# Kernel tuning notes

Measured on AMD Instinct MI355X. Metric: run time of the kernel, lower is better.

The kernel has to match this reference:

```python
import jax, jax.numpy as jnp
import numpy as np

BLANK = 0          # tf.nn.ctc_loss default blank_index (StringLookup reserves 0 for OOV)
PAD = 127          # padding_value = char_to_num.vocabulary_size()
NEG = -1e30        # log-space 'zero' (avoid -inf to keep grads NaN-free)
B, T, C, L = 1024, 256, 128, 32


def setup_inputs() -> dict:
    key = jax.random.key(0)
    k1, k2 = jax.random.split(key)
    # labels in [1, PAD-1]; none equal PAD so label_length == L (full-length labels)
    y_true = jax.random.randint(k1, (B, L), 1, PAD).astype(jnp.int32)
    y_pred = jax.random.normal(k2, (B, T, C), dtype=jnp.float32)
    return {"y_true": y_true, "y_pred": y_pred}


def _ctc_loss(y_true, y_pred):
    """Faithful jax version of tf.nn.ctc_loss(labels, logits, label_len, T,
    logits_time_major=False, blank_index=0): standard log-space alpha DP."""
    Bn, Tn, Cn = y_pred.shape
    Ln = y_true.shape[1]
    S = 2 * Ln + 1  # extended label length (blanks interleaved)

    logp = jax.nn.log_softmax(y_pred, axis=-1)                    # [B,T,C]

    # extended label sequence: blank, l1, blank, l2, ..., blank   # [B,S]
    ext = jnp.full((Bn, S), BLANK, dtype=y_true.dtype)
    ext = ext.at[:, 1::2].set(y_true)

    # log-probs gathered at extended-label symbols                # [B,T,S]
    lp_ext = jnp.take_along_axis(
        logp, jnp.broadcast_to(ext[:, None, :], (Bn, Tn, S)), axis=2)

    # label_length = count of non-padding entries (mirrors count_nonzero)
    label_len = jnp.sum(y_true != PAD, axis=1)                    # [B]

    # skip transition s-2 -> s allowed iff ext[s] is a non-blank differing
    # from ext[s-2]
    skip_ok = jnp.concatenate(
        [jnp.zeros((Bn, 2), bool),
         (ext[:, 2:] != BLANK) & (ext[:, 2:] != ext[:, :-2])], axis=1)  # [B,S]

    neg1 = jnp.full((Bn, 1), NEG, logp.dtype)
    neg2 = jnp.full((Bn, 2), NEG, logp.dtype)

    alpha0 = jnp.full((Bn, S), NEG, logp.dtype)
    alpha0 = alpha0.at[:, 0].set(lp_ext[:, 0, 0]).at[:, 1].set(lp_ext[:, 0, 1])

    def step(alpha, lp_t):  # alpha,[B,S]  lp_t,[B,S]
        a1 = jnp.concatenate([neg1, alpha[:, :-1]], axis=1)
        a2 = jnp.concatenate([neg2, alpha[:, :-2]], axis=1)
        a2 = jnp.where(skip_ok, a2, NEG)
        new = lp_t + jnp.logaddexp(jnp.logaddexp(alpha, a1), a2)
        return new, None

    lp_seq = jnp.transpose(lp_ext, (1, 0, 2))                     # [T,B,S]
    alphaT, _ = jax.lax.scan(step, alpha0, lp_seq[1:])            # [B,S]

    # total log-likelihood ends at last blank (2*len) or last label (2*len-1)
    bi = jnp.arange(Bn)
    e1 = 2 * label_len
    e2 = 2 * label_len - 1
    loglik = jnp.logaddexp(alphaT[bi, e1], alphaT[bi, e2])        # [B]
    return -loglik


def reference(y_true, y_pred):
    # The original layer returns y_pred and registers the loss via add_loss;
    # the compute-dominant quantity is the per-example CTC loss, returned here.
    return _ctc_loss(y_true, y_pred)
```

## Files before the change

kernel.cpp:

```cpp
#include <hip/hip_runtime.h>
#include <cstdint>


#define CTC_BLANK 0
#define CTC_PAD   127
#define NEG       (-1e30f)
#define LOG2E     1.44269504088896340736f
#define LN2       0.69314718055994530942f

constexpr int Bn = 1024, Tn = 256, Cn = 128, Ln = 32;
constexpr int NSLOT = Ln + 1;
constexpr int CR  = 16;
constexpr int NCH = Tn / CR;

__device__ __forceinline__ float fexp2(float x) { return __builtin_amdgcn_exp2f(x); }
__device__ __forceinline__ float flog2(float x) { return __builtin_amdgcn_logf(x); }

template <int CTRL>
__device__ __forceinline__ float dpp_add(float s) {
    int v = __builtin_amdgcn_update_dpp(0, __float_as_int(s), CTRL, 0xF, 0xF, true);
    return s + __int_as_float(v);
}
__device__ __forceinline__ float dpp_wave_shr1(float src, float old) {
    return __int_as_float(__builtin_amdgcn_update_dpp(
        __float_as_int(old), __float_as_int(src), 0x138, 0xF, 0xF, false));
}
__device__ __forceinline__ void gl_lds16(const float* g, float* l) {
    __builtin_amdgcn_global_load_lds(
        (const __attribute__((address_space(1))) uint32_t*)g,
        (__attribute__((address_space(3))) uint32_t*)l, 16, 0, 0);
}

__global__ __launch_bounds__(512, 8) void ctc_fused_kernel(
        const int*   __restrict__ y_true,
        const float* __restrict__ y_pred,
        float*       __restrict__ out)
{
    __shared__ __align__(16) float raw[8][2][CR / 8 * Cn];
    __shared__ _Float16 Gc[Tn * NSLOT];
    __shared__ int   labels[Ln];
    __shared__ __align__(16) int cmap[Cn];
    __shared__ int   used[Cn];
    __shared__ int   wcnt[8];
    __shared__ float partS[16];

    const int b    = blockIdx.x;
    const int tid  = threadIdx.x;
    const int lane = tid & 63;
    const int wave = tid >> 6;

    const float* gbase = y_pred + (size_t)b * Tn * Cn;

    auto stage = [&](int c, int buf) {
        const float* g = gbase + (size_t)(c * CR + 2 * wave) * Cn + lane * 4;
        gl_lds16(g, &raw[wave][buf][0]);
    };

    stage(0, 0);

    if (tid < Ln) labels[tid] = y_true[b * Ln + tid];
    if (tid < Cn) used[tid] = 0;
    __syncthreads();
    if (tid == 0) used[CTC_BLANK] = 1;
    if (tid < Ln) used[labels[tid]] = 1;
    __syncthreads();
    {
        bool f = (tid < Cn) && (used[tid] != 0);
        unsigned long long m = __ballot(f);
        if (lane == 0) wcnt[wave] = __popcll(m);
        __syncthreads();
        int base = 0;
        for (int w = 0; w < wave; ++w) base += wcnt[w];
        if (tid < Cn)
            cmap[tid] = f ? (base + __popcll(m & ((1ull << lane) - 1ull))) : -1;
        __syncthreads();
    }

    const int half = lane >> 5;
    const int l32  = lane & 31;
    const int4 cm  = ((const int4*)cmap)[l32];
    float acc = 0.f;

    for (int c = 0; c < NCH; ++c) {
        const float4 x = ((const float4*)&raw[wave][c & 1][0])[lane];
        if (c + 1 < NCH) stage(c + 1, (c + 1) & 1);

        const int r = c * CR + 2 * wave + half;
        if (cm.x >= 0) Gc[r * NSLOT + cm.x] = (_Float16)(x.x * LOG2E);
        if (cm.y >= 0) Gc[r * NSLOT + cm.y] = (_Float16)(x.y * LOG2E);
        if (cm.z >= 0) Gc[r * NSLOT + cm.z] = (_Float16)(x.z * LOG2E);
        if (cm.w >= 0) Gc[r * NSLOT + cm.w] = (_Float16)(x.w * LOG2E);
        float s = __expf(x.x) + __expf(x.y) + __expf(x.z) + __expf(x.w);
        s = dpp_add<0x111>(s);
        s = dpp_add<0x112>(s);
        s = dpp_add<0x114>(s);
        s = dpp_add<0x118>(s);
        s = dpp_add<0x142>(s);
        acc += __logf(s);
    }
    if (l32 == 31) partS[wave * 2 + half] = acc;
    __syncthreads();

    if (wave == 0) {
        const int  i      = lane;
        const bool validO = (i < Ln);
        const bool validE = (i <= Ln);
        const int  myLab   = validO ? labels[i] : -1;
        const int  prevLab = (i >= 1 && i < Ln) ? labels[i - 1] : -1;
        const int  slotO   = validO ? cmap[myLab] : 0;
        const bool skipO   = (i >= 1 && i < Ln) &&
                             (myLab != CTC_BLANK) && (myLab != prevLab);
        const int  len = __popcll(__ballot(validO && (myLab != CTC_PAD)));

        float aE = (i == 0) ? (float)Gc[0]     : NEG;
        float aO = (i == 0) ? (float)Gc[slotO] : NEG;

        float pB[2], pO[2];
        pB[0] = (float)Gc[NSLOT];     pO[0] = (float)Gc[NSLOT + slotO];
        pB[1] = (float)Gc[2 * NSLOT]; pO[1] = (float)Gc[2 * NSLOT + slotO];
        int k = 0;
        #pragma unroll 2
        for (int t = 1; t < Tn; ++t) {
            const float lpB = pB[k], lpO = pO[k];
            const int tp = (t + 2 < Tn) ? t + 2 : Tn - 1;
            pB[k] = (float)Gc[tp * NSLOT];
            pO[k] = (float)Gc[tp * NSLOT + slotO];
            k ^= 1;

            const float aOup = dpp_wave_shr1(aO, NEG);
            const float m  = fmaxf(aE, aOup);
            const float e1 = fexp2(aE - m);
            const float e2 = fexp2(aOup - m);
            const float sE = e1 + e2;
            const float nE = lpB + m + flog2(sE);
            const float m3 = fmaxf(aO, m);
            const float nO = lpO + m3 +
                flog2(fexp2(aO - m3) + (skipO ? sE : e1) * fexp2(m - m3));
            aE = validE ? nE : NEG;
            aO = validO ? nO : NEG;
        }

        const float v1 = __shfl(aE, len, 64);
        const float v2 = __shfl(aO, len - 1, 64);
        if (i == 0) {
            float S = 0.f;
            #pragma unroll
            for (int j = 0; j < 16; ++j) S += partS[j];
            const float mm = fmaxf(v1, v2);
            const float L2 = mm + flog2(fexp2(v1 - mm) + fexp2(v2 - mm));
            out[b] = S - LN2 * L2;
        }
    }
}

extern "C" void kernel_launch(void* const* d_in, const int* in_sizes, int n_in,
                              void* d_out, int out_size, void* d_ws, size_t ws_size,
                              hipStream_t stream) {
    const int*   y_true = (const int*)d_in[0];
    const float* y_pred = (const float*)d_in[1];
    float*       out    = (float*)d_out;
    ctc_fused_kernel<<<Bn, 512, 0, stream>>>(y_true, y_pred, out);
}
```

Before: 222.6 us.

## Split CTC into a parallel staging kernel and a single-wave DP kernel

Splits the fused kernel in two. The first kernel computes the log-sum-exp and gathers the compact fp16 label-column table, using 2 blocks of 256 threads per batch item, and writes the table and partial sums to workspace. The second kernel uses one 64-thread wave per batch item to load the table and run the serial alpha recursion. The DP kernel is small, so many more of them fit on a CU, which should let the 255-step serial chain overlap across batches instead of leaving 7 of 8 waves idle. The cost is an extra launch and a workspace round trip. The fused kernel stays as a fallback, now with plain global loads instead of async LDS staging.

```diff
diff --git a/kernel.cpp b/kernel.cpp
--- a/kernel.cpp
+++ b/kernel.cpp
@@ -10,8 +10,10 @@
 
 constexpr int Bn = 1024, Tn = 256, Cn = 128, Ln = 32;
 constexpr int NSLOT = Ln + 1;
-constexpr int CR  = 16;
-constexpr int NCH = Tn / CR;
+constexpr size_t GC_HALFS  = (size_t)Tn * NSLOT;
+constexpr size_t WS_GC_B   = (size_t)Bn * GC_HALFS * 2;
+constexpr size_t WS_S_B    = (size_t)Bn * 16 * 4;
+constexpr size_t WS_NEEDED = WS_GC_B + WS_S_B;
 
 __device__ __forceinline__ float fexp2(float x) { return __builtin_amdgcn_exp2f(x); }
 __device__ __forceinline__ float flog2(float x) { return __builtin_amdgcn_logf(x); }
@@ -25,38 +27,24 @@
     return __int_as_float(__builtin_amdgcn_update_dpp(
         __float_as_int(old), __float_as_int(src), 0x138, 0xF, 0xF, false));
 }
-__device__ __forceinline__ void gl_lds16(const float* g, float* l) {
-    __builtin_amdgcn_global_load_lds(
-        (const __attribute__((address_space(1))) uint32_t*)g,
-        (__attribute__((address_space(3))) uint32_t*)l, 16, 0, 0);
-}
-
-__global__ __launch_bounds__(512, 8) void ctc_fused_kernel(
+
+__global__ __launch_bounds__(256) void ctc_stage_kernel(
         const int*   __restrict__ y_true,
         const float* __restrict__ y_pred,
-        float*       __restrict__ out)
+        _Float16*    __restrict__ gws,
+        float*       __restrict__ sws)
 {
-    __shared__ __align__(16) float raw[8][2][CR / 8 * Cn];
-    __shared__ _Float16 Gc[Tn * NSLOT];
-    __shared__ int   labels[Ln];
+    __shared__ _Float16 Gt[128 * NSLOT];
+    __shared__ int labels[Ln];
     __shared__ __align__(16) int cmap[Cn];
-    __shared__ int   used[Cn];
-    __shared__ int   wcnt[8];
-    __shared__ float partS[16];
-
-    const int b    = blockIdx.x;
+    __shared__ int used[Cn];
+    __shared__ int wcnt[4];
+
+    const int h    = blockIdx.x;
+    const int b    = blockIdx.y;
     const int tid  = threadIdx.x;
     const int lane = tid & 63;
     const int wave = tid >> 6;
-
-    const float* gbase = y_pred + (size_t)b * Tn * Cn;
-
-    auto stage = [&](int c, int buf) {
-        const float* g = gbase + (size_t)(c * CR + 2 * wave) * Cn + lane * 4;
-        gl_lds16(g, &raw[wave][buf][0]);
-    };
-
-    stage(0, 0);
 
     if (tid < Ln) labels[tid] = y_true[b * Ln + tid];
     if (tid < Cn) used[tid] = 0;
@@ -76,16 +64,188 @@
         __syncthreads();
     }
 
+    const float* rowbase = y_pred + ((size_t)b * Tn + h * 128) * Cn;
     const int half = lane >> 5;
     const int l32  = lane & 31;
     const int4 cm  = ((const int4*)cmap)[l32];
     float acc = 0.f;
 
-    for (int c = 0; c < NCH; ++c) {
-        const float4 x = ((const float4*)&raw[wave][c & 1][0])[lane];
-        if (c + 1 < NCH) stage(c + 1, (c + 1) & 1);
-
-        const int r = c * CR + 2 * wave + half;
+    float4 v[2][4];
+    #pragma unroll
+    for (int j = 0; j < 4; ++j) {
+        const int rl = 2 * (wave * 16 + j) + half;
+        v[0][j] = ((const float4*)(rowbase + rl * Cn))[l32];
+    }
+    for (int g = 0; g < 4; ++g) {
+        if (g < 3) {
+            #pragma unroll
+            for (int j = 0; j < 4; ++j) {
+                const int rl = 2 * (wave * 16 + (g + 1) * 4 + j) + half;
+                v[(g + 1) & 1][j] = ((const float4*)(rowbase + rl * Cn))[l32];
+            }
+        }
+        #pragma unroll
+        for (int j = 0; j < 4; ++j) {
+            const float4 x = v[g & 1][j];
+            const int rl = 2 * (wave * 16 + g * 4 + j) + half;
+            if (cm.x >= 0) Gt[rl * NSLOT + cm.x] = (_Float16)(x.x * LOG2E);
+            if (cm.y >= 0) Gt[rl * NSLOT + cm.y] = (_Float16)(x.y * LOG2E);
+            if (cm.z >= 0) Gt[rl * NSLOT + cm.z] = (_Float16)(x.z * LOG2E);
+            if (cm.w >= 0) Gt[rl * NSLOT + cm.w] = (_Float16)(x.w * LOG2E);
+            float s = __expf(x.x) + __expf(x.y) + __expf(x.z) + __expf(x.w);
+            s = dpp_add<0x111>(s);
+            s = dpp_add<0x112>(s);
+            s = dpp_add<0x114>(s);
+            s = dpp_add<0x118>(s);
+            s = dpp_add<0x142>(s);
+            acc += __logf(s);
+        }
+    }
+    if (l32 == 31) sws[b * 16 + h * 8 + wave * 2 + half] = acc;
+    __syncthreads();
+
+    {
+        uint4*       dst = (uint4*)(gws + ((size_t)b * Tn + h * 128) * NSLOT);
+        const uint4* src = (const uint4*)Gt;
+        dst[tid]       = src[tid];
+        dst[256 + tid] = src[256 + tid];
+        if (tid < 16) dst[512 + tid] = src[512 + tid];
+    }
+}
+
+__global__ __launch_bounds__(64) void ctc_dp_kernel(
+        const int*      __restrict__ y_true,
+        const _Float16* __restrict__ gws,
+        const float*    __restrict__ sws,
+        float*          __restrict__ out)
+{
+    __shared__ __align__(16) _Float16 Gc[GC_HALFS];
+    __shared__ int labels[Ln];
+    __shared__ int used[Cn];
+    __shared__ int cmap[Cn];
+
+    const int b    = blockIdx.x;
+    const int lane = threadIdx.x;
+
+    {
+        const uint4* src = (const uint4*)(gws + (size_t)b * GC_HALFS);
+        uint4*       dst = (uint4*)Gc;
+        #pragma unroll
+        for (int k = 0; k < 17; ++k) {
+            const int idx = k * 64 + lane;
+            if (idx < 1056) dst[idx] = src[idx];
+        }
+    }
+
+    if (lane < Ln) labels[lane] = y_true[b * Ln + lane];
+    used[lane] = 0; used[64 + lane] = 0;
+    __syncthreads();
+    if (lane == 0) used[CTC_BLANK] = 1;
+    if (lane < Ln) used[labels[lane]] = 1;
+    __syncthreads();
+    {
+        const unsigned long long below = (1ull << lane) - 1ull;
+        const unsigned long long m0 = __ballot(used[lane] != 0);
+        const unsigned long long m1 = __ballot(used[64 + lane] != 0);
+        cmap[lane]      = used[lane]      ? (int)__popcll(m0 & below) : -1;
+        cmap[64 + lane] = used[64 + lane] ? (int)(__popcll(m0) +
+                                                  __popcll(m1 & below)) : -1;
+    }
+    __syncthreads();
+
+    const int  i      = lane;
+    const bool validO = (i < Ln);
+    const bool validE = (i <= Ln);
+    const int  myLab   = validO ? labels[i] : -1;
+    const int  prevLab = (i >= 1 && i < Ln) ? labels[i - 1] : -1;
+    const int  slotO   = validO ? cmap[myLab] : 0;
+    const bool skipO   = (i >= 1 && i < Ln) &&
+                         (myLab != CTC_BLANK) && (myLab != prevLab);
+    const int  len = __popcll(__ballot(validO && (myLab != CTC_PAD)));
+
+    float aE = (i == 0) ? (float)Gc[0]     : NEG;
+    float aO = (i == 0) ? (float)Gc[slotO] : NEG;
+
+    float pB[2], pO[2];
+    pB[0] = (float)Gc[NSLOT];     pO[0] = (float)Gc[NSLOT + slotO];
+    pB[1] = (float)Gc[2 * NSLOT]; pO[1] = (float)Gc[2 * NSLOT + slotO];
+    int k = 0;
+    #pragma unroll 2
+    for (int t = 1; t < Tn; ++t) {
+        const float lpB = pB[k], lpO = pO[k];
+        const int tp = (t + 2 < Tn) ? t + 2 : Tn - 1;
+        pB[k] = (float)Gc[tp * NSLOT];
+        pO[k] = (float)Gc[tp * NSLOT + slotO];
+        k ^= 1;
+
+        const float aOup = dpp_wave_shr1(aO, NEG);
+        const float m  = fmaxf(aE, aOup);
+        const float e1 = fexp2(aE - m);
+        const float e2 = fexp2(aOup - m);
+        const float sE = e1 + e2;
+        const float nE = lpB + m + flog2(sE);
+        const float m3 = fmaxf(aO, m);
+        const float nO = lpO + m3 +
+            flog2(fexp2(aO - m3) + (skipO ? sE : e1) * fexp2(m - m3));
+        aE = validE ? nE : NEG;
+        aO = validO ? nO : NEG;
+    }
+
+    const float v1 = __shfl(aE, len, 64);
+    const float v2 = __shfl(aO, len - 1, 64);
+    if (i == 0) {
+        float S = 0.f;
+        #pragma unroll
+        for (int j = 0; j < 16; ++j) S += sws[b * 16 + j];
+        const float mm = fmaxf(v1, v2);
+        const float L2 = mm + flog2(fexp2(v1 - mm) + fexp2(v2 - mm));
+        out[b] = S - LN2 * L2;
+    }
+}
+
+__global__ __launch_bounds__(512, 8) void ctc_fused_kernel(
+        const int*   __restrict__ y_true,
+        const float* __restrict__ y_pred,
+        float*       __restrict__ out)
+{
+    __shared__ _Float16 Gc[Tn * NSLOT];
+    __shared__ int   labels[Ln];
+    __shared__ __align__(16) int cmap[Cn];
+    __shared__ int   used[Cn];
+    __shared__ int   wcnt[8];
+    __shared__ float partS[16];
+
+    const int b    = blockIdx.x;
+    const int tid  = threadIdx.x;
+    const int lane = tid & 63;
+    const int wave = tid >> 6;
+
+    if (tid < Ln) labels[tid] = y_true[b * Ln + tid];
+    if (tid < Cn) used[tid] = 0;
+    __syncthreads();
+    if (tid == 0) used[CTC_BLANK] = 1;
+    if (tid < Ln) used[labels[tid]] = 1;
+    __syncthreads();
+    {
+        bool f = (tid < Cn) && (used[tid] != 0);
+        unsigned long long m = __ballot(f);
+        if (lane == 0) wcnt[wave] = __popcll(m);
+        __syncthreads();
+        int base = 0;
+        for (int w = 0; w < wave; ++w) base += wcnt[w];
+        if (tid < Cn)
+            cmap[tid] = f ? (base + __popcll(m & ((1ull << lane) - 1ull))) : -1;
+        __syncthreads();
+    }
+
+    const float* rowbase = y_pred + (size_t)b * Tn * Cn;
+    const int half = lane >> 5;
+    const int l32  = lane & 31;
+    const int4 cm  = ((const int4*)cmap)[l32];
+    float acc = 0.f;
+    for (int c = 0; c < 16; ++c) {
+        const int r = c * 16 + 2 * wave + half;
+        const float4 x = ((const float4*)(rowbase + r * Cn))[l32];
         if (cm.x >= 0) Gc[r * NSLOT + cm.x] = (_Float16)(x.x * LOG2E);
         if (cm.y >= 0) Gc[r * NSLOT + cm.y] = (_Float16)(x.y * LOG2E);
         if (cm.z >= 0) Gc[r * NSLOT + cm.z] = (_Float16)(x.z * LOG2E);
@@ -114,7 +274,6 @@
 
         float aE = (i == 0) ? (float)Gc[0]     : NEG;
         float aO = (i == 0) ? (float)Gc[slotO] : NEG;
-
         float pB[2], pO[2];
         pB[0] = (float)Gc[NSLOT];     pO[0] = (float)Gc[NSLOT + slotO];
         pB[1] = (float)Gc[2 * NSLOT]; pO[1] = (float)Gc[2 * NSLOT + slotO];
@@ -126,7 +285,6 @@
             pB[k] = (float)Gc[tp * NSLOT];
             pO[k] = (float)Gc[tp * NSLOT + slotO];
             k ^= 1;
-
             const float aOup = dpp_wave_shr1(aO, NEG);
             const float m  = fmaxf(aE, aOup);
             const float e1 = fexp2(aE - m);
@@ -139,7 +297,6 @@
             aE = validE ? nE : NEG;
             aO = validO ? nO : NEG;
         }
-
         const float v1 = __shfl(aE, len, 64);
         const float v2 = __shfl(aO, len - 1, 64);
         if (i == 0) {
@@ -159,5 +316,12 @@
     const int*   y_true = (const int*)d_in[0];
     const float* y_pred = (const float*)d_in[1];
     float*       out    = (float*)d_out;
-    ctc_fused_kernel<<<Bn, 512, 0, stream>>>(y_true, y_pred, out);
-}
+    if (ws_size >= WS_NEEDED) {
+        _Float16* gws = (_Float16*)d_ws;
+        float*    sws = (float*)((char*)d_ws + WS_GC_B);
+        ctc_stage_kernel<<<dim3(2, Bn), 256, 0, stream>>>(y_true, y_pred, gws, sws);
+        ctc_dp_kernel<<<Bn, 64, 0, stream>>>(y_true, gws, sws, out);
+    } else {
+        ctc_fused_kernel<<<Bn, 512, 0, stream>>>(y_true, y_pred, out);
+    }
+}
```

Measured after the change: 219.9 us. No clear change (-1.2%).
